# Performance work log

Hardware: AMD Instinct MI355X
Metric: run time of the kernel (lower is better)

Reference implementation:

```python
import jax, jax.numpy as jnp
import numpy as np

B, S, D, H = 2, 2048, 1024, 16


def setup_inputs() -> dict:
    key = jax.random.key(0)
    kq, kk, kv, kw = jax.random.split(key, 4)
    Q = jax.random.normal(kq, (B, S, D), dtype=jnp.float32)
    K = jax.random.normal(kk, (B, S, D), dtype=jnp.float32)
    V = jax.random.normal(kv, (B, S, D), dtype=jnp.float32)
    Wo = jax.random.normal(kw, (D, D), dtype=jnp.float32) * (1.0 / np.sqrt(D))
    return {"Q": Q, "K": K, "V": V, "Wo": Wo, "num_heads": H}


def reference(Q, K, V, Wo, num_heads):
    b, s, d = Q.shape
    dk = d // num_heads
    # split heads: [B,S,D] -> [B,H,S,dk]
    q = Q.reshape(b, s, num_heads, dk).transpose(0, 2, 1, 3)
    k = K.reshape(b, s, num_heads, dk).transpose(0, 2, 1, 3)
    v = V.reshape(b, s, num_heads, dk).transpose(0, 2, 1, 3)
    scale = 1.0 / jnp.sqrt(jnp.asarray(dk, dtype=q.dtype))
    logits = jnp.einsum('bhqd,bhkd->bhqk', q, k) * scale  # [B,H,S,S]
    probs = jax.nn.softmax(logits, axis=-1).astype(q.dtype)
    o = jnp.einsum('bhqk,bhkd->bhqd', probs, v)  # [B,H,S,dk]
    o = o.transpose(0, 2, 1, 3).reshape(b, s, d)  # concat heads
    # O = einsum('d dkh, ... dkh -> ... d', Wo, scores) == scores @ Wo^T
    return jnp.einsum('dk,bsk->bsd', Wo, o)
```

## Files before the change

kernel.cpp:

```cpp
#include <hip/hip_runtime.h>
#include <hip/hip_bf16.h>

#define B_ 2
#define S_ 2048
#define D_ 1024
#define H_ 16
#define DK_ 64

typedef __hip_bfloat16 bf16;
typedef short v8s __attribute__((ext_vector_type(8)));
typedef short v4s __attribute__((ext_vector_type(4)));
typedef float v4f __attribute__((ext_vector_type(4)));
typedef float v16f __attribute__((ext_vector_type(16)));
typedef int   v4i __attribute__((ext_vector_type(4)));
typedef int   v2i __attribute__((ext_vector_type(2)));

static __device__ __forceinline__ v16f mfma32(v8s a, v8s b, v16f c) {
  return __builtin_amdgcn_mfma_f32_32x32x16_bf16(a, b, c, 0, 0, 0);
}
static __device__ __forceinline__ void gl2lds16(const void* g, void* l) {
  __builtin_amdgcn_global_load_lds((const __attribute__((address_space(1))) void*)g,
                                   (__attribute__((address_space(3))) void*)l,
                                   16, 0, 0);
}
static __device__ __forceinline__ short f2bf(float x) {
  return (short)__builtin_bit_cast(unsigned short, __float2bfloat16(x));
}
static __device__ __forceinline__ int pk2f(float lo, float hi) {
  unsigned a = __builtin_bit_cast(unsigned, lo) + 0x8000u;
  unsigned b = __builtin_bit_cast(unsigned, hi) + 0x8000u;
  return (int)__builtin_amdgcn_perm(b, a, 0x07060302u);
}
static __device__ __forceinline__ float bf2f(short s) {
  return __builtin_bit_cast(float, ((unsigned)(unsigned short)s) << 16);
}

__global__ __launch_bounds__(256) void pre_kernel(
    const float* __restrict__ K, const float* __restrict__ V,
    const float* __restrict__ Wo, bf16* __restrict__ Kb,
    bf16* __restrict__ Vt, bf16* __restrict__ Wb)
{
  __shared__ __align__(16) bf16 td[64 * 72];
  const int t = threadIdx.x;
  const int bx = blockIdx.x;

  if (bx < 2048) {
    const int idx = bx * 256 + t;
    const int seg = idx & 7;
    const int rest = idx >> 3;
    const int h = rest & 15;
    const int bs = rest >> 4;
    const float* src = K + (size_t)bs * D_ + h * 64 + seg * 8;
    v4f x = *(const v4f*)src, y = *(const v4f*)(src + 4);
    v8s r;
    r[0]=f2bf(x[0]); r[1]=f2bf(x[1]); r[2]=f2bf(x[2]); r[3]=f2bf(x[3]);
    r[4]=f2bf(y[0]); r[5]=f2bf(y[1]); r[6]=f2bf(y[2]); r[7]=f2bf(y[3]);
    const int b = bs >> 11, s = bs & 2047;
    *(v8s*)(Kb + ((size_t)(b * H_ + h) * S_ + s) * DK_ + seg * 8) = r;
  } else if (bx < 3072) {
    const int idx = bx - 2048;
    const int bh = idx >> 5, b = bh >> 4, h = bh & 15;
    const int s0 = (idx & 31) * 64;
    const int srow = t >> 2;
    const int cs = t & 3;
    const float* vp = V + (size_t)(b * S_ + s0 + srow) * D_ + h * 64 + cs * 16;
#pragma unroll
    for (int j = 0; j < 4; j++) {
      v4f x = *(const v4f*)(vp + j * 4);
#pragma unroll
      for (int jj = 0; jj < 4; jj++)
        td[(cs * 16 + j * 4 + jj) * 72 + srow] = __float2bfloat16(x[jj]);
    }
    __syncthreads();
    const int d = t >> 2;
#pragma unroll
    for (int a2 = 0; a2 < 4; a2++) {
      const int pos = cs * 16 + a2 * 4;
      const int g = pos >> 5;
      const int a = (pos >> 2) & 7;
      const int kbase = g * 32 + ((a >> 2) << 4) + ((a & 1) << 3) + (((a >> 1) & 1) << 2);
      v4s val = *(const v4s*)(td + d * 72 + kbase);
      *(v4s*)(Vt + ((size_t)bh * DK_ + d) * S_ + s0 + pos) = val;
    }
  } else {
    const int i = ((bx - 3072) * 256 + t) * 4;
    v4f a = *(const v4f*)(Wo + i);
    v4s r;
    r[0]=f2bf(a[0]); r[1]=f2bf(a[1]); r[2]=f2bf(a[2]); r[3]=f2bf(a[3]);
    *(v4s*)((short*)Wb + i) = r;
  }
}

__global__ __launch_bounds__(256, 4) void attn4_kernel(
    const float* __restrict__ Q, const bf16* __restrict__ Kb,
    const bf16* __restrict__ Vt, bf16* __restrict__ Op0,
    bf16* __restrict__ Op1, float* __restrict__ Lp)
{
  __shared__ __align__(16) bf16 kk[2][64 * 64];
  __shared__ __align__(16) bf16 vv[2][64 * 64];

  const int t = threadIdx.x;
  const int w = t >> 6, l = t & 63, h2 = l >> 5, ln = l & 31;
  const int bh = blockIdx.x, b = bh >> 4, h = bh & 15;
  const int qbase = blockIdx.y * 128 + w * 32;
  const int z = blockIdx.z;
  const int kb0 = z << 10;

  const bf16* Kbh = Kb + (size_t)bh * (S_ * DK_);
  const bf16* Vbh = Vt + (size_t)bh * (DK_ * S_);

  const float sc = 0.18033688011112042f;
  v8s bq[4];
  {
    const float* qp = Q + ((size_t)b * S_ + qbase + ln) * D_ + h * DK_ + h2 * 8;
#pragma unroll
    for (int c = 0; c < 4; c++) {
      v4f x = *(const v4f*)(qp + c * 16);
      v4f y = *(const v4f*)(qp + c * 16 + 4);
      v4i r = { pk2f(x[0]*sc, x[1]*sc), pk2f(x[2]*sc, x[3]*sc),
                pk2f(y[0]*sc, y[1]*sc), pk2f(y[2]*sc, y[3]*sc) };
      bq[c] = __builtin_bit_cast(v8s, r);
    }
  }

  v16f accA, accB;
#pragma unroll
  for (int r = 0; r < 16; r++) { accA[r] = 0.f; accB[r] = 0.f; }
  float lpart = 0.f;

#pragma unroll
  for (int j = 0; j < 2; j++) {
    const int flat = j * 256 + t, row = flat >> 3, sp = flat & 7;
    gl2lds16(Kbh + (size_t)(kb0 + row) * DK_ + ((sp ^ (row & 7)) * 8), &kk[0][flat * 8]);
    gl2lds16(Vbh + (size_t)row * S_ + kb0 + ((sp ^ (row & 7)) * 8), &vv[0][flat * 8]);
  }

  int it = 0;
  for (int kb = kb0; kb < kb0 + 1024; kb += 64, it ^= 1) {
    __syncthreads();
    if (kb + 64 < kb0 + 1024) {
#pragma unroll
      for (int j = 0; j < 2; j++) {
        const int flat = j * 256 + t, row = flat >> 3, sp = flat & 7;
        gl2lds16(Kbh + (size_t)(kb + 64 + row) * DK_ + ((sp ^ (row & 7)) * 8),
                 &kk[it ^ 1][flat * 8]);
        gl2lds16(Vbh + (size_t)row * S_ + (kb + 64) + ((sp ^ (row & 7)) * 8),
                 &vv[it ^ 1][flat * 8]);
      }
    }
    const bf16* kc_ = kk[it];
    const bf16* vc_ = vv[it];

    v16f s0, s1;
#pragma unroll
    for (int r = 0; r < 16; r++) { s0[r] = 0.f; s1[r] = 0.f; }
#pragma unroll
    for (int c = 0; c < 4; c++) {
      const int sd = 2 * c + h2;
      v8s a0 = *(const v8s*)(kc_ + ln * 64 + ((sd ^ (ln & 7)) * 8));
      v8s a1 = *(const v8s*)(kc_ + (32 + ln) * 64 + ((sd ^ (ln & 7)) * 8));
      s0 = mfma32(a0, bq[c], s0);
      s1 = mfma32(a1, bq[c], s1);
    }

    float p0[16], p1[16];
#pragma unroll
    for (int r = 0; r < 16; r++) { p0[r] = exp2f(s0[r]); p1[r] = exp2f(s1[r]); }
    float su = 0.f;
#pragma unroll
    for (int r = 0; r < 16; r++) su += p0[r] + p1[r];
    lpart += su;

    v4i i00 = { pk2f(p0[0],p0[1]),  pk2f(p0[2],p0[3]),  pk2f(p0[4],p0[5]),  pk2f(p0[6],p0[7]) };
    v4i i01 = { pk2f(p0[8],p0[9]),  pk2f(p0[10],p0[11]),pk2f(p0[12],p0[13]),pk2f(p0[14],p0[15]) };
    v4i i10 = { pk2f(p1[0],p1[1]),  pk2f(p1[2],p1[3]),  pk2f(p1[4],p1[5]),  pk2f(p1[6],p1[7]) };
    v4i i11 = { pk2f(p1[8],p1[9]),  pk2f(p1[10],p1[11]),pk2f(p1[12],p1[13]),pk2f(p1[14],p1[15]) };
    v8s pb00 = __builtin_bit_cast(v8s, i00);
    v8s pb01 = __builtin_bit_cast(v8s, i01);
    v8s pb10 = __builtin_bit_cast(v8s, i10);
    v8s pb11 = __builtin_bit_cast(v8s, i11);

#pragma unroll
    for (int st = 0; st < 2; st++) {
#pragma unroll
      for (int kc = 0; kc < 2; kc++) {
        const int q = st * 4 + kc * 2 + h2;
        v8s avA = *(const v8s*)(vc_ + ln * 64 + ((q ^ (ln & 7)) * 8));
        v8s avB = *(const v8s*)(vc_ + (32 + ln) * 64 + ((q ^ (ln & 7)) * 8));
        v8s pb = st ? (kc ? pb11 : pb10) : (kc ? pb01 : pb00);
        accA = mfma32(avA, pb, accA);
        accB = mfma32(avB, pb, accB);
      }
    }
  }

  __syncthreads();
  const float lfull = lpart + __shfl_xor(lpart, 32);
  const float linv = 1.0f / lfull;
  bf16* epw = &kk[0][0] + w * 2048;
#pragma unroll
  for (int r = 0; r < 16; r += 4) {
    const int off = 4 * h2;
    const int sgA = (r >> 2) ^ (ln & 3);
    const int sgB = 4 + sgA;
    v2i pa = { pk2f(accA[r]*linv,   accA[r+1]*linv),
               pk2f(accA[r+2]*linv, accA[r+3]*linv) };
    v2i pb = { pk2f(accB[r]*linv,   accB[r+1]*linv),
               pk2f(accB[r+2]*linv, accB[r+3]*linv) };
    *(v2i*)(epw + ln * 64 + sgA * 8 + off) = pa;
    *(v2i*)(epw + ln * 64 + sgB * 8 + off) = pb;
  }
  if (h2 == 0)
    Lp[((size_t)z * 32 + bh) * S_ + qbase + ln] = lfull;

  bf16* Op = z ? Op1 : Op0;
#pragma unroll
  for (int i = 0; i < 4; i++) {
    const int flat = i * 64 + l;
    const int qr = flat >> 3, sd = flat & 7;
    const int phys = ((sd & 3) ^ (qr & 3)) | (sd & 4);
    v8s val = *(const v8s*)(epw - w * 2048 + (w * 32 + qr) * 64 + phys * 8);
    *(v8s*)(Op + ((size_t)b * S_ + qbase - w * 32 + w * 32 + qr) * D_ + h * DK_ + sd * 8) = val;
  }
}

__global__ __launch_bounds__(256) void merge_kernel(
    const bf16* __restrict__ Op0, const bf16* __restrict__ Op1,
    const float* __restrict__ Lp, bf16* __restrict__ O)
{
  const int flat = blockIdx.x * 256 + threadIdx.x;
  const int qrow = flat >> 7;
  const int seg = flat & 127;
  const int b = qrow >> 11, s = qrow & 2047;
  const int h = seg >> 3;
  const int bh = b * H_ + h;
  const float l0 = Lp[(size_t)bh * S_ + s];
  const float l1 = Lp[(size_t)(32 + bh) * S_ + s];
  const float inv = 1.0f / (l0 + l1);
  const float w0 = l0 * inv, w1 = l1 * inv;
  const size_t off = (size_t)qrow * D_ + seg * 8;
  v8s a = *(const v8s*)(Op0 + off);
  v8s c = *(const v8s*)(Op1 + off);
  v4i r;
#pragma unroll
  for (int j = 0; j < 4; j++) {
    float lo = w0 * bf2f(a[2*j])   + w1 * bf2f(c[2*j]);
    float hi = w0 * bf2f(a[2*j+1]) + w1 * bf2f(c[2*j+1]);
    r[j] = pk2f(lo, hi);
  }
  *(v8s*)(O + off) = __builtin_bit_cast(v8s, r);
}

__global__ __launch_bounds__(256, 4) void proj3_kernel(
    const bf16* __restrict__ A, const bf16* __restrict__ Wo, float* __restrict__ Out)
{
  __shared__ __align__(16) bf16 aa[2][64 * 64];
  __shared__ __align__(16) bf16 bb[2][64 * 64];

  const int t = threadIdx.x;
  const int w = t >> 6, l = t & 63, h2 = l >> 5, ln = l & 31;
  const int m0 = blockIdx.x * 64, n0 = blockIdx.y * 64;
  const int wm = (w & 1) * 32, wn = (w >> 1) * 32;

  v16f acc;
#pragma unroll
  for (int r = 0; r < 16; r++) acc[r] = 0.f;

#pragma unroll
  for (int j = 0; j < 2; j++) {
    const int flat = j * 256 + t, row = flat >> 3, sp = flat & 7;
    gl2lds16(A  + (size_t)(m0 + row) * D_ + ((sp ^ (row & 7)) * 8), &aa[0][flat * 8]);
    gl2lds16(Wo + (size_t)(n0 + row) * D_ + ((sp ^ (row & 7)) * 8), &bb[0][flat * 8]);
  }

  int it = 0;
  for (int k0 = 0; k0 < D_; k0 += 64, it ^= 1) {
    __syncthreads();
    if (k0 + 64 < D_) {
#pragma unroll
      for (int j = 0; j < 2; j++) {
        const int flat = j * 256 + t, row = flat >> 3, sp = flat & 7;
        gl2lds16(A  + (size_t)(m0 + row) * D_ + (k0 + 64) + ((sp ^ (row & 7)) * 8),
                 &aa[it ^ 1][flat * 8]);
        gl2lds16(Wo + (size_t)(n0 + row) * D_ + (k0 + 64) + ((sp ^ (row & 7)) * 8),
                 &bb[it ^ 1][flat * 8]);
      }
    }
    const bf16* ac = aa[it];
    const bf16* bc = bb[it];
#pragma unroll
    for (int c = 0; c < 4; c++) {
      const int sd = 2 * c + h2;
      v8s av = *(const v8s*)(ac + (wm + ln) * 64 + ((sd ^ (ln & 7)) * 8));
      v8s bv = *(const v8s*)(bc + (wn + ln) * 64 + ((sd ^ (ln & 7)) * 8));
      acc = mfma32(av, bv, acc);
    }
  }

#pragma unroll
  for (int r = 0; r < 16; r++) {
    const int row = m0 + wm + (r & 3) + 4 * h2 + 8 * (r >> 2);
    Out[(size_t)row * D_ + n0 + wn + ln] = acc[r];
  }
}

extern "C" void kernel_launch(void* const* d_in, const int* in_sizes, int n_in,
                              void* d_out, int out_size, void* d_ws, size_t ws_size,
                              hipStream_t stream) {
  (void)in_sizes; (void)n_in; (void)out_size; (void)ws_size;
  const float* Q  = (const float*)d_in[0];
  const float* K  = (const float*)d_in[1];
  const float* V  = (const float*)d_in[2];
  const float* Wo = (const float*)d_in[3];
  float* out = (float*)d_out;

  bf16* base = (bf16*)d_ws;
  bf16* kb   = base;
  bf16* vt   = base + (size_t)4  * 1024 * 1024;
  bf16* wo_b = base + (size_t)8  * 1024 * 1024;
  bf16* op0  = base + (size_t)9  * 1024 * 1024;
  bf16* op1  = base + (size_t)13 * 1024 * 1024;
  float* lp  = (float*)(base + (size_t)17 * 1024 * 1024);
  bf16* ows  = kb;

  pre_kernel  <<<dim3(4096),       256, 0, stream>>>(K, V, Wo, kb, vt, wo_b);
  attn4_kernel<<<dim3(32, 16, 2),  256, 0, stream>>>(Q, kb, vt, op0, op1, lp);
  merge_kernel<<<dim3(2048),       256, 0, stream>>>(op0, op1, lp, ows);
  proj3_kernel<<<dim3(64, 16),     256, 0, stream>>>(ows, wo_b, out);
}
```

Before: 176.8 us.

## Fuse split-KV merge into projection and shrink attention blocks to two waves

The separate merge kernel is removed. Its weighted combination of the two split-KV partial outputs now happens inside the projection kernel while it stages the A tile into LDS, so the combined bf16 activation is never written to and re-read from global memory. The attention kernel is also rebuilt as 128-thread blocks that each cover 64 query rows and walk 32-key tiles, which doubles the grid and allows more resident blocks per CU. The costs: every projection column block recomputes the merge for its rows (16 times redundant, with extra Op0/Op1 traffic that L2 should mostly serve), and the attention loop runs twice as many barriers with half the MFMA work per step.

New measurement: 194.9 us. +10.2%, slower.

```diff
diff --git a/kernel.cpp b/kernel.cpp
--- a/kernel.cpp
+++ b/kernel.cpp
@@ -91,18 +91,18 @@
   }
 }
 
-__global__ __launch_bounds__(256, 4) void attn4_kernel(
+__global__ __launch_bounds__(128, 8) void attn5_kernel(
     const float* __restrict__ Q, const bf16* __restrict__ Kb,
     const bf16* __restrict__ Vt, bf16* __restrict__ Op0,
     bf16* __restrict__ Op1, float* __restrict__ Lp)
 {
-  __shared__ __align__(16) bf16 kk[2][64 * 64];
-  __shared__ __align__(16) bf16 vv[2][64 * 64];
+  __shared__ __align__(16) bf16 kk[2][32 * 64];
+  __shared__ __align__(16) bf16 vv[2][64 * 32];
 
   const int t = threadIdx.x;
   const int w = t >> 6, l = t & 63, h2 = l >> 5, ln = l & 31;
   const int bh = blockIdx.x, b = bh >> 4, h = bh & 15;
-  const int qbase = blockIdx.y * 128 + w * 32;
+  const int qbase = blockIdx.y * 64 + w * 32;
   const int z = blockIdx.z;
   const int kb0 = z << 10;
 
@@ -130,67 +130,60 @@
 
 #pragma unroll
   for (int j = 0; j < 2; j++) {
-    const int flat = j * 256 + t, row = flat >> 3, sp = flat & 7;
-    gl2lds16(Kbh + (size_t)(kb0 + row) * DK_ + ((sp ^ (row & 7)) * 8), &kk[0][flat * 8]);
-    gl2lds16(Vbh + (size_t)row * S_ + kb0 + ((sp ^ (row & 7)) * 8), &vv[0][flat * 8]);
+    const int fk = j * 128 + t, rk = fk >> 3, sk = fk & 7;
+    gl2lds16(Kbh + (size_t)(kb0 + rk) * DK_ + ((sk ^ (rk & 7)) * 8), &kk[0][fk * 8]);
+    const int fv = j * 128 + t, dv = fv >> 2, sv = fv & 3;
+    gl2lds16(Vbh + (size_t)dv * S_ + kb0 + ((sv ^ (dv & 3)) * 8), &vv[0][fv * 8]);
   }
 
   int it = 0;
-  for (int kb = kb0; kb < kb0 + 1024; kb += 64, it ^= 1) {
+  for (int kb = kb0; kb < kb0 + 1024; kb += 32, it ^= 1) {
     __syncthreads();
-    if (kb + 64 < kb0 + 1024) {
+    if (kb + 32 < kb0 + 1024) {
 #pragma unroll
       for (int j = 0; j < 2; j++) {
-        const int flat = j * 256 + t, row = flat >> 3, sp = flat & 7;
-        gl2lds16(Kbh + (size_t)(kb + 64 + row) * DK_ + ((sp ^ (row & 7)) * 8),
-                 &kk[it ^ 1][flat * 8]);
-        gl2lds16(Vbh + (size_t)row * S_ + (kb + 64) + ((sp ^ (row & 7)) * 8),
-                 &vv[it ^ 1][flat * 8]);
+        const int fk = j * 128 + t, rk = fk >> 3, sk = fk & 7;
+        gl2lds16(Kbh + (size_t)(kb + 32 + rk) * DK_ + ((sk ^ (rk & 7)) * 8),
+                 &kk[it ^ 1][fk * 8]);
+        const int fv = j * 128 + t, dv = fv >> 2, sv = fv & 3;
+        gl2lds16(Vbh + (size_t)dv * S_ + (kb + 32) + ((sv ^ (dv & 3)) * 8),
+                 &vv[it ^ 1][fv * 8]);
       }
     }
     const bf16* kc_ = kk[it];
     const bf16* vc_ = vv[it];
 
-    v16f s0, s1;
-#pragma unroll
-    for (int r = 0; r < 16; r++) { s0[r] = 0.f; s1[r] = 0.f; }
+    v16f s;
+#pragma unroll
+    for (int r = 0; r < 16; r++) s[r] = 0.f;
 #pragma unroll
     for (int c = 0; c < 4; c++) {
       const int sd = 2 * c + h2;
       v8s a0 = *(const v8s*)(kc_ + ln * 64 + ((sd ^ (ln & 7)) * 8));
-      v8s a1 = *(const v8s*)(kc_ + (32 + ln) * 64 + ((sd ^ (ln & 7)) * 8));
-      s0 = mfma32(a0, bq[c], s0);
-      s1 = mfma32(a1, bq[c], s1);
-    }
-
-    float p0[16], p1[16];
-#pragma unroll
-    for (int r = 0; r < 16; r++) { p0[r] = exp2f(s0[r]); p1[r] = exp2f(s1[r]); }
+      s = mfma32(a0, bq[c], s);
+    }
+
+    float p[16];
+#pragma unroll
+    for (int r = 0; r < 16; r++) p[r] = exp2f(s[r]);
     float su = 0.f;
 #pragma unroll
-    for (int r = 0; r < 16; r++) su += p0[r] + p1[r];
+    for (int r = 0; r < 16; r++) su += p[r];
     lpart += su;
 
-    v4i i00 = { pk2f(p0[0],p0[1]),  pk2f(p0[2],p0[3]),  pk2f(p0[4],p0[5]),  pk2f(p0[6],p0[7]) };
-    v4i i01 = { pk2f(p0[8],p0[9]),  pk2f(p0[10],p0[11]),pk2f(p0[12],p0[13]),pk2f(p0[14],p0[15]) };
-    v4i i10 = { pk2f(p1[0],p1[1]),  pk2f(p1[2],p1[3]),  pk2f(p1[4],p1[5]),  pk2f(p1[6],p1[7]) };
-    v4i i11 = { pk2f(p1[8],p1[9]),  pk2f(p1[10],p1[11]),pk2f(p1[12],p1[13]),pk2f(p1[14],p1[15]) };
-    v8s pb00 = __builtin_bit_cast(v8s, i00);
-    v8s pb01 = __builtin_bit_cast(v8s, i01);
-    v8s pb10 = __builtin_bit_cast(v8s, i10);
-    v8s pb11 = __builtin_bit_cast(v8s, i11);
-
-#pragma unroll
-    for (int st = 0; st < 2; st++) {
-#pragma unroll
-      for (int kc = 0; kc < 2; kc++) {
-        const int q = st * 4 + kc * 2 + h2;
-        v8s avA = *(const v8s*)(vc_ + ln * 64 + ((q ^ (ln & 7)) * 8));
-        v8s avB = *(const v8s*)(vc_ + (32 + ln) * 64 + ((q ^ (ln & 7)) * 8));
-        v8s pb = st ? (kc ? pb11 : pb10) : (kc ? pb01 : pb00);
-        accA = mfma32(avA, pb, accA);
-        accB = mfma32(avB, pb, accB);
-      }
+    v4i i0 = { pk2f(p[0],p[1]),  pk2f(p[2],p[3]),  pk2f(p[4],p[5]),  pk2f(p[6],p[7]) };
+    v4i i1 = { pk2f(p[8],p[9]),  pk2f(p[10],p[11]),pk2f(p[12],p[13]),pk2f(p[14],p[15]) };
+    v8s pb0 = __builtin_bit_cast(v8s, i0);
+    v8s pb1 = __builtin_bit_cast(v8s, i1);
+
+#pragma unroll
+    for (int kc = 0; kc < 2; kc++) {
+      const int q = kc * 2 + h2;
+      v8s avA = *(const v8s*)(vc_ + ln * 32 + ((q ^ (ln & 3)) * 8));
+      v8s avB = *(const v8s*)(vc_ + (32 + ln) * 32 + ((q ^ (ln & 3)) * 8));
+      v8s pb = kc ? pb1 : pb0;
+      accA = mfma32(avA, pb, accA);
+      accB = mfma32(avB, pb, accB);
     }
   }
 
@@ -214,45 +207,21 @@
     Lp[((size_t)z * 32 + bh) * S_ + qbase + ln] = lfull;
 
   bf16* Op = z ? Op1 : Op0;
+  __syncthreads();
 #pragma unroll
   for (int i = 0; i < 4; i++) {
     const int flat = i * 64 + l;
     const int qr = flat >> 3, sd = flat & 7;
     const int phys = ((sd & 3) ^ (qr & 3)) | (sd & 4);
-    v8s val = *(const v8s*)(epw - w * 2048 + (w * 32 + qr) * 64 + phys * 8);
-    *(v8s*)(Op + ((size_t)b * S_ + qbase - w * 32 + w * 32 + qr) * D_ + h * DK_ + sd * 8) = val;
-  }
-}
-
-__global__ __launch_bounds__(256) void merge_kernel(
+    v8s val = *(const v8s*)(epw + qr * 64 + phys * 8);
+    *(v8s*)(Op + ((size_t)b * S_ + qbase + qr) * D_ + h * DK_ + sd * 8) = val;
+  }
+}
+
+__global__ __launch_bounds__(256, 4) void proj4_kernel(
     const bf16* __restrict__ Op0, const bf16* __restrict__ Op1,
-    const float* __restrict__ Lp, bf16* __restrict__ O)
-{
-  const int flat = blockIdx.x * 256 + threadIdx.x;
-  const int qrow = flat >> 7;
-  const int seg = flat & 127;
-  const int b = qrow >> 11, s = qrow & 2047;
-  const int h = seg >> 3;
-  const int bh = b * H_ + h;
-  const float l0 = Lp[(size_t)bh * S_ + s];
-  const float l1 = Lp[(size_t)(32 + bh) * S_ + s];
-  const float inv = 1.0f / (l0 + l1);
-  const float w0 = l0 * inv, w1 = l1 * inv;
-  const size_t off = (size_t)qrow * D_ + seg * 8;
-  v8s a = *(const v8s*)(Op0 + off);
-  v8s c = *(const v8s*)(Op1 + off);
-  v4i r;
-#pragma unroll
-  for (int j = 0; j < 4; j++) {
-    float lo = w0 * bf2f(a[2*j])   + w1 * bf2f(c[2*j]);
-    float hi = w0 * bf2f(a[2*j+1]) + w1 * bf2f(c[2*j+1]);
-    r[j] = pk2f(lo, hi);
-  }
-  *(v8s*)(O + off) = __builtin_bit_cast(v8s, r);
-}
-
-__global__ __launch_bounds__(256, 4) void proj3_kernel(
-    const bf16* __restrict__ A, const bf16* __restrict__ Wo, float* __restrict__ Out)
+    const float* __restrict__ Lp, const bf16* __restrict__ Wo,
+    float* __restrict__ Out)
 {
   __shared__ __align__(16) bf16 aa[2][64 * 64];
   __shared__ __align__(16) bf16 bb[2][64 * 64];
@@ -262,29 +231,56 @@
   const int m0 = blockIdx.x * 64, n0 = blockIdx.y * 64;
   const int wm = (w & 1) * 32, wn = (w >> 1) * 32;
 
+  const int arow = t >> 2;
+  const int aph = t & 3;
+  const int qrow = m0 + arow;
+  const int b = qrow >> 11, s = qrow & 2047;
+
   v16f acc;
 #pragma unroll
   for (int r = 0; r < 16; r++) acc[r] = 0.f;
 
-#pragma unroll
-  for (int j = 0; j < 2; j++) {
-    const int flat = j * 256 + t, row = flat >> 3, sp = flat & 7;
-    gl2lds16(A  + (size_t)(m0 + row) * D_ + ((sp ^ (row & 7)) * 8), &aa[0][flat * 8]);
-    gl2lds16(Wo + (size_t)(n0 + row) * D_ + ((sp ^ (row & 7)) * 8), &bb[0][flat * 8]);
-  }
+  auto stageA = [&](int k0, int buf) {
+    const int h = k0 >> 6;
+    const float l0 = Lp[(size_t)(b * H_ + h) * S_ + s];
+    const float l1 = Lp[(size_t)(32 + b * H_ + h) * S_ + s];
+    const float inv = 1.0f / (l0 + l1);
+    const float w0 = l0 * inv, w1 = l1 * inv;
+#pragma unroll
+    for (int jj = 0; jj < 2; jj++) {
+      const int ph = aph + jj * 4;
+      const int logical = ph ^ (arow & 7);
+      const size_t off = (size_t)qrow * D_ + k0 + logical * 8;
+      v8s a8 = *(const v8s*)(Op0 + off);
+      v8s c8 = *(const v8s*)(Op1 + off);
+      v4i r;
+#pragma unroll
+      for (int j = 0; j < 4; j++) {
+        float lo = w0 * bf2f(a8[2*j])   + w1 * bf2f(c8[2*j]);
+        float hi = w0 * bf2f(a8[2*j+1]) + w1 * bf2f(c8[2*j+1]);
+        r[j] = pk2f(lo, hi);
+      }
+      *(v8s*)(&aa[buf][arow * 64 + ph * 8]) = __builtin_bit_cast(v8s, r);
+    }
+  };
+  auto stageB = [&](int k0, int buf) {
+#pragma unroll
+    for (int j = 0; j < 2; j++) {
+      const int flat = j * 256 + t, row = flat >> 3, sp = flat & 7;
+      gl2lds16(Wo + (size_t)(n0 + row) * D_ + k0 + ((sp ^ (row & 7)) * 8),
+               &bb[buf][flat * 8]);
+    }
+  };
+
+  stageA(0, 0);
+  stageB(0, 0);
 
   int it = 0;
   for (int k0 = 0; k0 < D_; k0 += 64, it ^= 1) {
     __syncthreads();
     if (k0 + 64 < D_) {
-#pragma unroll
-      for (int j = 0; j < 2; j++) {
-        const int flat = j * 256 + t, row = flat >> 3, sp = flat & 7;
-        gl2lds16(A  + (size_t)(m0 + row) * D_ + (k0 + 64) + ((sp ^ (row & 7)) * 8),
-                 &aa[it ^ 1][flat * 8]);
-        gl2lds16(Wo + (size_t)(n0 + row) * D_ + (k0 + 64) + ((sp ^ (row & 7)) * 8),
-                 &bb[it ^ 1][flat * 8]);
-      }
+      stageA(k0 + 64, it ^ 1);
+      stageB(k0 + 64, it ^ 1);
     }
     const bf16* ac = aa[it];
     const bf16* bc = bb[it];
@@ -321,10 +317,8 @@
   bf16* op0  = base + (size_t)9  * 1024 * 1024;
   bf16* op1  = base + (size_t)13 * 1024 * 1024;
   float* lp  = (float*)(base + (size_t)17 * 1024 * 1024);
-  bf16* ows  = kb;
 
   pre_kernel  <<<dim3(4096),       256, 0, stream>>>(K, V, Wo, kb, vt, wo_b);
-  attn4_kernel<<<dim3(32, 16, 2),  256, 0, stream>>>(Q, kb, vt, op0, op1, lp);
-  merge_kernel<<<dim3(2048),       256, 0, stream>>>(op0, op1, lp, ows);
-  proj3_kernel<<<dim3(64, 16),     256, 0, stream>>>(ows, wo_b, out);
-}
+  attn5_kernel<<<dim3(32, 32, 2),  128, 0, stream>>>(Q, kb, vt, op0, op1, lp);
+  proj4_kernel<<<dim3(64, 16),     256, 0, stream>>>(op0, op1, lp, wo_b, out);
+}
```

## Enlarge output-projection GEMM tile to 128x128 with 2x2 MFMA per wave

Applied to the files above, without the earlier changes.

The output projection kernel now computes 128x128 tiles per block, with each wave holding four 32x32 accumulators, so every LDS fragment load is reused across two MFMAs. This reduces LDS and global traffic per FLOP. In exchange it raises register and LDS use and cuts the grid to 256 blocks. The attention row-sum is split into four independent partial sums to shorten the dependency chain, and the epilogue adds a barrier with simplified indexing.

Result: no change. 178.1 us (+0.7%).

```diff
diff --git a/kernel.cpp b/kernel.cpp
--- a/kernel.cpp
+++ b/kernel.cpp
@@ -166,10 +166,13 @@
     float p0[16], p1[16];
 #pragma unroll
     for (int r = 0; r < 16; r++) { p0[r] = exp2f(s0[r]); p1[r] = exp2f(s1[r]); }
-    float su = 0.f;
-#pragma unroll
-    for (int r = 0; r < 16; r++) su += p0[r] + p1[r];
-    lpart += su;
+    float sa = 0.f, sb = 0.f, sc2 = 0.f, sd2 = 0.f;
+#pragma unroll
+    for (int r = 0; r < 16; r += 4) {
+      sa += p0[r];     sb += p0[r + 1];  sc2 += p0[r + 2]; sd2 += p0[r + 3];
+      sa += p1[r];     sb += p1[r + 1];  sc2 += p1[r + 2]; sd2 += p1[r + 3];
+    }
+    lpart += (sa + sb) + (sc2 + sd2);
 
     v4i i00 = { pk2f(p0[0],p0[1]),  pk2f(p0[2],p0[3]),  pk2f(p0[4],p0[5]),  pk2f(p0[6],p0[7]) };
     v4i i01 = { pk2f(p0[8],p0[9]),  pk2f(p0[10],p0[11]),pk2f(p0[12],p0[13]),pk2f(p0[14],p0[15]) };
@@ -214,12 +217,13 @@
     Lp[((size_t)z * 32 + bh) * S_ + qbase + ln] = lfull;
 
   bf16* Op = z ? Op1 : Op0;
+  __syncthreads();
 #pragma unroll
   for (int i = 0; i < 4; i++) {
     const int flat = i * 64 + l;
     const int qr = flat >> 3, sd = flat & 7;
     const int phys = ((sd & 3) ^ (qr & 3)) | (sd & 4);
-    v8s val = *(const v8s*)(epw - w * 2048 + (w * 32 + qr) * 64 + phys * 8);
+    v8s val = *(const v8s*)(epw + qr * 64 + phys * 8);
     *(v8s*)(Op + ((size_t)b * S_ + qbase - w * 32 + w * 32 + qr) * D_ + h * DK_ + sd * 8) = val;
   }
 }
@@ -251,23 +255,27 @@
   *(v8s*)(O + off) = __builtin_bit_cast(v8s, r);
 }
 
-__global__ __launch_bounds__(256, 4) void proj3_kernel(
+__global__ __launch_bounds__(256, 2) void proj6_kernel(
     const bf16* __restrict__ A, const bf16* __restrict__ Wo, float* __restrict__ Out)
 {
-  __shared__ __align__(16) bf16 aa[2][64 * 64];
-  __shared__ __align__(16) bf16 bb[2][64 * 64];
+  __shared__ __align__(16) bf16 aa[2][128 * 64];
+  __shared__ __align__(16) bf16 bb[2][128 * 64];
 
   const int t = threadIdx.x;
   const int w = t >> 6, l = t & 63, h2 = l >> 5, ln = l & 31;
-  const int m0 = blockIdx.x * 64, n0 = blockIdx.y * 64;
-  const int wm = (w & 1) * 32, wn = (w >> 1) * 32;
-
-  v16f acc;
-#pragma unroll
-  for (int r = 0; r < 16; r++) acc[r] = 0.f;
-
-#pragma unroll
-  for (int j = 0; j < 2; j++) {
+  const int m0 = blockIdx.x * 128, n0 = blockIdx.y * 128;
+  const int wm = (w & 1) * 64, wn = (w >> 1) * 64;
+
+  v16f acc[2][2];
+#pragma unroll
+  for (int mi = 0; mi < 2; mi++)
+#pragma unroll
+    for (int ni = 0; ni < 2; ni++)
+#pragma unroll
+      for (int r = 0; r < 16; r++) acc[mi][ni][r] = 0.f;
+
+#pragma unroll
+  for (int j = 0; j < 4; j++) {
     const int flat = j * 256 + t, row = flat >> 3, sp = flat & 7;
     gl2lds16(A  + (size_t)(m0 + row) * D_ + ((sp ^ (row & 7)) * 8), &aa[0][flat * 8]);
     gl2lds16(Wo + (size_t)(n0 + row) * D_ + ((sp ^ (row & 7)) * 8), &bb[0][flat * 8]);
@@ -278,7 +286,7 @@
     __syncthreads();
     if (k0 + 64 < D_) {
 #pragma unroll
-      for (int j = 0; j < 2; j++) {
+      for (int j = 0; j < 4; j++) {
         const int flat = j * 256 + t, row = flat >> 3, sp = flat & 7;
         gl2lds16(A  + (size_t)(m0 + row) * D_ + (k0 + 64) + ((sp ^ (row & 7)) * 8),
                  &aa[it ^ 1][flat * 8]);
@@ -289,19 +297,32 @@
     const bf16* ac = aa[it];
     const bf16* bc = bb[it];
 #pragma unroll
-    for (int c = 0; c < 4; c++) {
-      const int sd = 2 * c + h2;
-      v8s av = *(const v8s*)(ac + (wm + ln) * 64 + ((sd ^ (ln & 7)) * 8));
-      v8s bv = *(const v8s*)(bc + (wn + ln) * 64 + ((sd ^ (ln & 7)) * 8));
-      acc = mfma32(av, bv, acc);
-    }
-  }
-
-#pragma unroll
-  for (int r = 0; r < 16; r++) {
-    const int row = m0 + wm + (r & 3) + 4 * h2 + 8 * (r >> 2);
-    Out[(size_t)row * D_ + n0 + wn + ln] = acc[r];
-  }
+    for (int kc = 0; kc < 4; kc++) {
+      const int sd = 2 * kc + h2;
+      v8s am[2], bn[2];
+#pragma unroll
+      for (int mi = 0; mi < 2; mi++)
+        am[mi] = *(const v8s*)(ac + (wm + mi * 32 + ln) * 64 + ((sd ^ (ln & 7)) * 8));
+#pragma unroll
+      for (int ni = 0; ni < 2; ni++)
+        bn[ni] = *(const v8s*)(bc + (wn + ni * 32 + ln) * 64 + ((sd ^ (ln & 7)) * 8));
+#pragma unroll
+      for (int mi = 0; mi < 2; mi++)
+#pragma unroll
+        for (int ni = 0; ni < 2; ni++)
+          acc[mi][ni] = mfma32(am[mi], bn[ni], acc[mi][ni]);
+    }
+  }
+
+#pragma unroll
+  for (int mi = 0; mi < 2; mi++)
+#pragma unroll
+    for (int ni = 0; ni < 2; ni++)
+#pragma unroll
+      for (int r = 0; r < 16; r++) {
+        const int row = m0 + wm + mi * 32 + (r & 3) + 4 * h2 + 8 * (r >> 2);
+        Out[(size_t)row * D_ + n0 + wn + ni * 32 + ln] = acc[mi][ni][r];
+      }
 }
 
 extern "C" void kernel_launch(void* const* d_in, const int* in_sizes, int n_in,
@@ -326,5 +347,5 @@
   pre_kernel  <<<dim3(4096),       256, 0, stream>>>(K, V, Wo, kb, vt, wo_b);
   attn4_kernel<<<dim3(32, 16, 2),  256, 0, stream>>>(Q, kb, vt, op0, op1, lp);
   merge_kernel<<<dim3(2048),       256, 0, stream>>>(op0, op1, lp, ows);
-  proj3_kernel<<<dim3(64, 16),     256, 0, stream>>>(ows, wo_b, out);
-}
+  proj6_kernel<<<dim3(32, 8),      256, 0, stream>>>(ows, wo_b, out);
+}
```
